# Optimization experiments

Measured on AMD Instinct MI355X. Metric: run time of the kernel, lower is better.

Reference implementation:

```python
import jax, jax.numpy as jnp
import numpy as np

D_MODEL = 1024
NUM_HEADS = 16


def setup_inputs() -> dict:
    key = jax.random.key(0)
    kx, kq, kk, kv, ko = jax.random.split(key, 5)
    B, S, D = 4, 2048, D_MODEL
    scale = 0.02
    x = jax.random.normal(kx, (B, S, D), dtype=jnp.float32)
    wq = jax.random.normal(kq, (D, D), dtype=jnp.float32) * scale
    wk = jax.random.normal(kk, (D, D), dtype=jnp.float32) * scale
    wv = jax.random.normal(kv, (D, D), dtype=jnp.float32) * scale
    wo = jax.random.normal(ko, (D, D), dtype=jnp.float32) * scale
    return {"x": x, "wq": wq, "wk": wk, "wv": wv, "wo": wo}


def reference(x, wq, wk, wv, wo):
    B, S, D = x.shape
    H = NUM_HEADS
    dk = D // H
    # projections: weight is [out, in] -> y = x @ W^T
    q = jnp.einsum('bsd,ed->bse', x, wq).reshape(B, S, H, dk).transpose(0, 2, 1, 3)
    k = jnp.einsum('bsd,ed->bse', x, wk).reshape(B, S, H, dk).transpose(0, 2, 1, 3)
    v = jnp.einsum('bsd,ed->bse', x, wv).reshape(B, S, H, dk).transpose(0, 2, 1, 3)
    # scaled dot-product attention with causal mask, [B,H,S,S]
    scores = jnp.einsum('bhqd,bhkd->bhqk', q, k) / jnp.sqrt(jnp.asarray(dk, x.dtype))
    causal = jnp.tril(jnp.ones((S, S), dtype=bool))
    scores = jnp.where(causal, scores, -jnp.inf)
    attn = jax.nn.softmax(scores, axis=-1)
    out = jnp.einsum('bhqk,bhkd->bhqd', attn, v)
    out = out.transpose(0, 2, 1, 3).reshape(B, S, D)
    return jnp.einsum('bse,de->bsd', out, wo)
```

## Files before the change

### kernel.cpp

```cpp
#include <hip/hip_runtime.h>

#define SEQ 2048
#define DM 1024
#define NH 16
#define DKH 64

typedef __attribute__((ext_vector_type(8))) short short8;
typedef __attribute__((ext_vector_type(4))) float f32x4;

static __device__ __forceinline__ unsigned short f2b(float f) {
  unsigned int u = __float_as_uint(f);
  u += 0x7fffu + ((u >> 16) & 1u);
  return (unsigned short)(u >> 16);
}

static __device__ __forceinline__ short8 ldfrag_bf(const unsigned short* p) {
  return *reinterpret_cast<const short8*>(p);
}
static __device__ __forceinline__ short8 ldfrag_f32(const float* p) {
  const float4* q = reinterpret_cast<const float4*>(p);
  float4 a = q[0], b = q[1];
  short8 r;
  r[0] = (short)f2b(a.x); r[1] = (short)f2b(a.y);
  r[2] = (short)f2b(a.z); r[3] = (short)f2b(a.w);
  r[4] = (short)f2b(b.x); r[5] = (short)f2b(b.y);
  r[6] = (short)f2b(b.z); r[7] = (short)f2b(b.w);
  return r;
}

static __device__ __forceinline__ void gl_lds16(const void* g, void* l) {
  __builtin_amdgcn_global_load_lds(
      (const __attribute__((address_space(1))) unsigned int*)g,
      (__attribute__((address_space(3))) unsigned int*)l, 16, 0, 0);
}

__global__ __launch_bounds__(256) void zero_f32(float* __restrict__ p, int n4) {
  int i = blockIdx.x * 256 + threadIdx.x;
  if (i < n4) {
    float4 z = {0.f, 0.f, 0.f, 0.f};
    reinterpret_cast<float4*>(p)[i] = z;
  }
}

__global__ __launch_bounds__(256) void cast_f32_bf16(const float* __restrict__ src,
                                                     unsigned short* __restrict__ dst,
                                                     int n4) {
  int i = blockIdx.x * 256 + threadIdx.x;
  if (i < n4) {
    float4 v = reinterpret_cast<const float4*>(src)[i];
    ushort4 o;
    o.x = f2b(v.x); o.y = f2b(v.y); o.z = f2b(v.z); o.w = f2b(v.w);
    reinterpret_cast<ushort4*>(dst)[i] = o;
  }
}

__global__ __launch_bounds__(256) void cast4_w(const float* __restrict__ a, const float* __restrict__ b,
                                               const float* __restrict__ c, const float* __restrict__ d,
                                               unsigned short* __restrict__ oa, unsigned short* __restrict__ ob,
                                               unsigned short* __restrict__ oc, unsigned short* __restrict__ od) {
  int which = blockIdx.x >> 10;
  int i = (blockIdx.x & 1023) * 256 + threadIdx.x;
  const float* s = (which == 0) ? a : (which == 1) ? b : (which == 2) ? c : d;
  unsigned short* o = (which == 0) ? oa : (which == 1) ? ob : (which == 2) ? oc : od;
  float sc = (which == 0) ? 0.125f : 1.0f;
  float4 v = reinterpret_cast<const float4*>(s)[i];
  ushort4 u;
  u.x = f2b(v.x * sc); u.y = f2b(v.y * sc); u.z = f2b(v.z * sc); u.w = f2b(v.w * sc);
  reinterpret_cast<ushort4*>(o)[i] = u;
}

__global__ __launch_bounds__(256) void gemm_qkv(const unsigned short* __restrict__ A,
                                                const unsigned short* __restrict__ Wq,
                                                const unsigned short* __restrict__ Wk,
                                                const unsigned short* __restrict__ Wv,
                                                unsigned short* __restrict__ Qb,
                                                unsigned short* __restrict__ Kb,
                                                unsigned short* __restrict__ Vt) {
  __shared__ char smem[32768];
  unsigned short* At = (unsigned short*)smem;
  unsigned short* Wt = (unsigned short*)(smem + 16384);
  int t = threadIdx.x;
  int lane = t & 63;
  int w = t >> 6;
  int l16 = lane & 15, q4 = lane >> 4;
  int mode = blockIdx.x % 3;
  int bid = blockIdx.x / 3;
  int mt = bid >> 3, nt = bid & 7;
  int m0 = mt * 128, n0 = nt * 128;
  int mw = (w & 1) * 64, nw = (w >> 1) * 64;
  const unsigned short* W = (mode == 0) ? Wq : (mode == 1) ? Wk : Wv;

  const f32x4 zero4 = {0.f, 0.f, 0.f, 0.f};
  f32x4 acc[4][4];
#pragma unroll
  for (int mi = 0; mi < 4; ++mi)
#pragma unroll
    for (int nj = 0; nj < 4; ++nj) acc[mi][nj] = zero4;

  int rl0 = t >> 2, cp = t & 3;
  const unsigned short* ga0 = A + (long)(m0 + rl0) * DM + ((cp - rl0) & 3) * 8;
  const unsigned short* ga1 = A + (long)(m0 + rl0 + 64) * DM + ((cp - (rl0 + 64)) & 3) * 8;
  const unsigned short* gw0 = W + (long)(n0 + rl0) * DM + ((cp - rl0) & 3) * 8;
  const unsigned short* gw1 = W + (long)(n0 + rl0 + 64) * DM + ((cp - (rl0 + 64)) & 3) * 8;
  char* lA = (char*)At + t * 16;
  char* lW = (char*)Wt + t * 16;

  int aoff[4], woff[4];
#pragma unroll
  for (int mi = 0; mi < 4; ++mi) {
    int r = mw + mi * 16 + l16;
    aoff[mi] = r * 32 + ((q4 + r) & 3) * 8;
  }
#pragma unroll
  for (int nj = 0; nj < 4; ++nj) {
    int r = nw + nj * 16 + l16;
    woff[nj] = r * 32 + ((q4 + r) & 3) * 8;
  }

  gl_lds16(ga0, lA); gl_lds16(ga1, lA + 4096);
  gl_lds16(gw0, lW); gl_lds16(gw1, lW + 4096);

  for (int ks = 0; ks < 32; ++ks) {
    __syncthreads();
    if (ks + 1 < 32) {
      ga0 += 32; ga1 += 32; gw0 += 32; gw1 += 32;
      int bo = ((ks + 1) & 1) * 8192;
      gl_lds16(ga0, lA + bo); gl_lds16(ga1, lA + bo + 4096);
      gl_lds16(gw0, lW + bo); gl_lds16(gw1, lW + bo + 4096);
    }
    const unsigned short* Ab = At + (ks & 1) * 4096;
    const unsigned short* Wb = Wt + (ks & 1) * 4096;

    short8 af[4], wf[4];
#pragma unroll
    for (int mi = 0; mi < 4; ++mi) af[mi] = ldfrag_bf(Ab + aoff[mi]);
#pragma unroll
    for (int nj = 0; nj < 4; ++nj) wf[nj] = ldfrag_bf(Wb + woff[nj]);
#pragma unroll
    for (int mi = 0; mi < 4; ++mi)
#pragma unroll
      for (int nj = 0; nj < 4; ++nj)
        acc[mi][nj] = __builtin_amdgcn_mfma_f32_16x16x32_bf16(af[mi], wf[nj], acc[mi][nj], 0, 0, 0);
  }

  if (mode != 2) {
    unsigned short* o = (mode == 0) ? Qb : Kb;
#pragma unroll
    for (int mi = 0; mi < 4; ++mi)
#pragma unroll
      for (int nj = 0; nj < 4; ++nj)
#pragma unroll
        for (int r = 0; r < 4; ++r) {
          int m = m0 + mw + mi * 16 + q4 * 4 + r;
          int n = n0 + nw + nj * 16 + l16;
          int b = m >> 11, s = m & 2047;
          int h = n >> 6, d = n & 63;
          long bh = (long)(b * NH + h);
          o[(bh * SEQ + s) * DKH + d] = f2b(acc[mi][nj][r]);
        }
  } else {
    __syncthreads();
    unsigned short* vle = (unsigned short*)(smem + w * 8192);
    unsigned int* vle32 = (unsigned int*)vle;
#pragma unroll
    for (int nj = 0; nj < 4; ++nj) {
      int d = nj * 16 + l16;
      int k8 = (d & 7) * 8;
#pragma unroll
      for (int mi = 0; mi < 4; ++mi)
#pragma unroll
        for (int r = 0; r < 4; r += 2) {
          int s = mi * 16 + q4 * 4 + r;
          unsigned int pk = (unsigned int)f2b(acc[mi][nj][r]) |
                            ((unsigned int)f2b(acc[mi][nj][r + 1]) << 16);
          vle32[d * 32 + ((s ^ k8) >> 1)] = pk;
        }
    }
    __asm__ volatile("s_waitcnt lgkmcnt(0)" ::: "memory");
    int b = m0 >> 11;
    int h = (n0 + nw) >> 6;
    long bh = (long)(b * NH + h);
    int sbase = (m0 + mw) & 2047;
    int dr_lo = lane >> 3, c = lane & 7;
#pragma unroll
    for (int pass = 0; pass < 8; ++pass) {
      int dr = pass * 8 + dr_lo;
      int cc = c ^ (dr & 7);
      short8 vv = ldfrag_bf(vle + dr * 64 + cc * 8);
      *reinterpret_cast<short8*>(Vt + (bh * DKH + dr) * SEQ + sbase + c * 8) = vv;
    }
  }
}

__global__ __launch_bounds__(256) void gemm_o(const unsigned short* __restrict__ A,
                                              const unsigned short* __restrict__ W,
                                              float* __restrict__ outp) {
  __shared__ char smem[32768];
  unsigned short* At = (unsigned short*)smem;
  unsigned short* Wt = (unsigned short*)(smem + 16384);
  int t = threadIdx.x;
  int lane = t & 63;
  int w = t >> 6;
  int l16 = lane & 15, q4 = lane >> 4;
  int mt = blockIdx.x >> 3, nt = blockIdx.x & 7;
  int m0 = mt * 128, n0 = nt * 128;
  int mw = (w & 1) * 64, nw = (w >> 1) * 64;

  const f32x4 zero4 = {0.f, 0.f, 0.f, 0.f};
  f32x4 acc[4][4];
#pragma unroll
  for (int mi = 0; mi < 4; ++mi)
#pragma unroll
    for (int nj = 0; nj < 4; ++nj) acc[mi][nj] = zero4;

  int rl0 = t >> 2, cp = t & 3;
  int b0 = m0 >> 11;
  const unsigned short* ga0;
  const unsigned short* ga1;
  {
    int s0 = (m0 & 2047) + rl0;
    ga0 = A + (long)b0 * (NH * SEQ * DKH) + (long)s0 * DKH + ((cp - rl0) & 3) * 8;
    int s1 = (m0 & 2047) + rl0 + 64;
    ga1 = A + (long)b0 * (NH * SEQ * DKH) + (long)s1 * DKH + ((cp - (rl0 + 64)) & 3) * 8;
  }
  const unsigned short* gw0 = W + (long)(n0 + rl0) * DM + ((cp - rl0) & 3) * 8;
  const unsigned short* gw1 = W + (long)(n0 + rl0 + 64) * DM + ((cp - (rl0 + 64)) & 3) * 8;
  char* lA = (char*)At + t * 16;
  char* lW = (char*)Wt + t * 16;

  int aoff[4], woff[4];
#pragma unroll
  for (int mi = 0; mi < 4; ++mi) {
    int r = mw + mi * 16 + l16;
    aoff[mi] = r * 32 + ((q4 + r) & 3) * 8;
  }
#pragma unroll
  for (int nj = 0; nj < 4; ++nj) {
    int r = nw + nj * 16 + l16;
    woff[nj] = r * 32 + ((q4 + r) & 3) * 8;
  }

  gl_lds16(ga0, lA); gl_lds16(ga1, lA + 4096);
  gl_lds16(gw0, lW); gl_lds16(gw1, lW + 4096);

  for (int ks = 0; ks < 32; ++ks) {
    __syncthreads();
    if (ks + 1 < 32) {
      int adv = ((ks & 1) == 0) ? 32 : (SEQ * DKH - 32);
      ga0 += adv; ga1 += adv; gw0 += 32; gw1 += 32;
      int bo = ((ks + 1) & 1) * 8192;
      gl_lds16(ga0, lA + bo); gl_lds16(ga1, lA + bo + 4096);
      gl_lds16(gw0, lW + bo); gl_lds16(gw1, lW + bo + 4096);
    }
    const unsigned short* Ab = At + (ks & 1) * 4096;
    const unsigned short* Wb = Wt + (ks & 1) * 4096;

    short8 af[4], wf[4];
#pragma unroll
    for (int mi = 0; mi < 4; ++mi) af[mi] = ldfrag_bf(Ab + aoff[mi]);
#pragma unroll
    for (int nj = 0; nj < 4; ++nj) wf[nj] = ldfrag_bf(Wb + woff[nj]);
#pragma unroll
    for (int mi = 0; mi < 4; ++mi)
#pragma unroll
      for (int nj = 0; nj < 4; ++nj)
        acc[mi][nj] = __builtin_amdgcn_mfma_f32_16x16x32_bf16(af[mi], wf[nj], acc[mi][nj], 0, 0, 0);
  }

#pragma unroll
  for (int mi = 0; mi < 4; ++mi)
#pragma unroll
    for (int nj = 0; nj < 4; ++nj)
#pragma unroll
      for (int r = 0; r < 4; ++r) {
        int m = m0 + mw + mi * 16 + q4 * 4 + r;
        int n = n0 + nw + nj * 16 + l16;
        outp[(long)m * DM + n] = acc[mi][nj][r];
      }
}

template<int MODE, bool AF32, bool WF32>
__global__ __launch_bounds__(256) void gemm_s(const void* __restrict__ Ap,
                                              const void* __restrict__ Wp,
                                              void* __restrict__ outp) {
  int wid  = (blockIdx.x * 256 + threadIdx.x) >> 6;
  int lane = threadIdx.x & 63;
  int l16  = lane & 15, q4 = lane >> 4;
  int tn = wid & 15, tm = wid >> 4;
  int m0 = tm * 32, n0 = tn * 64;

  const float*          Af = (const float*)Ap;
  const unsigned short* Ab = (const unsigned short*)Ap;
  const float*          Wf = (const float*)Wp;
  const unsigned short* Wb = (const unsigned short*)Wp;

  const f32x4 zero4 = {0.f, 0.f, 0.f, 0.f};
  f32x4 acc[2][4];
#pragma unroll
  for (int mi = 0; mi < 2; ++mi)
#pragma unroll
    for (int j = 0; j < 4; ++j) acc[mi][j] = zero4;

  int wrow[4];
#pragma unroll
  for (int j = 0; j < 4; ++j) wrow[j] = (n0 + j * 16 + l16) * DM;
  int arow[2] = {0, 0};
  long abase[2] = {0, 0};
  if (MODE != 3) {
#pragma unroll
    for (int mi = 0; mi < 2; ++mi) arow[mi] = (m0 + mi * 16 + l16) * DM;
  } else {
    int b = m0 >> 11;
#pragma unroll
    for (int mi = 0; mi < 2; ++mi) {
      int srow = (m0 & 2047) + mi * 16 + l16;
      abase[mi] = (long)b * (NH * SEQ * DKH) + (long)srow * DKH;
    }
  }

#pragma unroll 2
  for (int ks = 0; ks < 32; ++ks) {
    int ko = ks * 32 + q4 * 8;
    short8 bfrag[4];
#pragma unroll
    for (int j = 0; j < 4; ++j) {
      if constexpr (WF32) bfrag[j] = ldfrag_f32(Wf + wrow[j] + ko);
      else                bfrag[j] = ldfrag_bf(Wb + wrow[j] + ko);
    }
    short8 afrag[2];
    if constexpr (MODE != 3) {
#pragma unroll
      for (int mi = 0; mi < 2; ++mi) {
        if constexpr (AF32) afrag[mi] = ldfrag_f32(Af + arow[mi] + ko);
        else                afrag[mi] = ldfrag_bf(Ab + arow[mi] + ko);
      }
    } else {
      int h = ko >> 6, e63 = ko & 63;
#pragma unroll
      for (int mi = 0; mi < 2; ++mi)
        afrag[mi] = ldfrag_bf(Ab + abase[mi] + (long)h * (SEQ * DKH) + e63);
    }
#pragma unroll
    for (int mi = 0; mi < 2; ++mi)
#pragma unroll
      for (int j = 0; j < 4; ++j)
        acc[mi][j] = __builtin_amdgcn_mfma_f32_16x16x32_bf16(afrag[mi], bfrag[j], acc[mi][j], 0, 0, 0);
  }

#pragma unroll
  for (int mi = 0; mi < 2; ++mi) {
#pragma unroll
    for (int j = 0; j < 4; ++j) {
#pragma unroll
      for (int r = 0; r < 4; ++r) {
        float v = acc[mi][j][r];
        int m = m0 + mi * 16 + q4 * 4 + r;
        int n = n0 + j * 16 + l16;
        if constexpr (MODE == 3) {
          reinterpret_cast<float*>(outp)[(long)m * DM + n] = v;
        } else {
          int b = m >> 11, s = m & 2047;
          int h = n >> 6, d = n & 63;
          long bh = (long)(b * NH + h);
          unsigned short* o = reinterpret_cast<unsigned short*>(outp);
          if constexpr (MODE == 0)      o[(bh * SEQ + s) * DKH + d] = f2b(v * 0.125f);
          else if constexpr (MODE == 1) o[(bh * SEQ + s) * DKH + d] = f2b(v);
          else                          o[(bh * DKH + d) * SEQ + s] = f2b(v);
        }
      }
    }
  }
}

#define PSTR 72
__global__ __launch_bounds__(256) void attn_k(const unsigned short* __restrict__ Kbuf,
                                              const unsigned short* __restrict__ Vt,
                                              const unsigned short* __restrict__ Qbuf,
                                              unsigned short* __restrict__ Obuf) {
  __shared__ unsigned short Kt[2][64 * 64];
  __shared__ unsigned short Vts[2][64 * 64];
  __shared__ unsigned short Pl[4][32 * PSTR];

  int t = threadIdx.x;
  int lane = t & 63;
  int w = t >> 6;
  int l16 = lane & 15, q4 = lane >> 4;
  int qb = 15 - (blockIdx.x >> 6);
  int bh = blockIdx.x & 63;
  int q0 = qb * 128;
  int qw0 = q0 + w * 32;

  const unsigned short* Qh = Qbuf + (long)bh * (SEQ * DKH);
  const unsigned short* Kh = Kbuf + (long)bh * (SEQ * DKH);
  const unsigned short* Vh = Vt   + (long)bh * (DKH * SEQ);
  unsigned short* pl = Pl[w];

  short8 qf[2][2];
#pragma unroll
  for (int mi = 0; mi < 2; ++mi)
#pragma unroll
    for (int c = 0; c < 2; ++c)
      qf[mi][c] = ldfrag_bf(Qh + (qw0 + mi * 16 + l16) * DKH + c * 32 + q4 * 8);

  short8 onef;
#pragma unroll
  for (int j = 0; j < 8; ++j) onef[j] = (short)0x3F80;

  const f32x4 zero4 = {0.f, 0.f, 0.f, 0.f};
  f32x4 om[2][4], lsum[2];
#pragma unroll
  for (int mi = 0; mi < 2; ++mi) {
    lsum[mi] = zero4;
#pragma unroll
    for (int c = 0; c < 4; ++c) om[mi][c] = zero4;
  }

  int koff[4][2], voff[4][2];
#pragma unroll
  for (int tt = 0; tt < 4; ++tt) {
    int kr = tt * 16 + l16;
#pragma unroll
    for (int c = 0; c < 2; ++c) koff[tt][c] = kr * 64 + ((c * 4 + q4 + kr) & 7) * 8;
  }
#pragma unroll
  for (int c = 0; c < 4; ++c) {
    int dr = c * 16 + l16;
#pragma unroll
    for (int half = 0; half < 2; ++half) voff[c][half] = dr * 64 + ((half * 4 + q4 + dr) & 7) * 8;
  }

  int rl0 = t >> 3, cp = t & 7;
  const unsigned short* kp0 = Kh + (long)rl0 * DKH + ((cp - rl0) & 7) * 8;
  const unsigned short* kp1 = Kh + (long)(rl0 + 32) * DKH + ((cp - (rl0 + 32)) & 7) * 8;
  const unsigned short* vp0 = Vh + (long)rl0 * SEQ + ((cp - rl0) & 7) * 8;
  const unsigned short* vp1 = Vh + (long)(rl0 + 32) * SEQ + ((cp - (rl0 + 32)) & 7) * 8;
  char* lK = (char*)Kt + t * 16;
  char* lV = (char*)Vts + t * 16;

  int nk = 2 * qb + 2;
  gl_lds16(kp0, lK); gl_lds16(kp1, lK + 4096);
  gl_lds16(vp0, lV); gl_lds16(vp1, lV + 4096);

  for (int it = 0; it < nk; ++it) {
    __syncthreads();
    if (it + 1 < nk) {
      kp0 += 64 * DKH; kp1 += 64 * DKH; vp0 += 64; vp1 += 64;
      int bo = ((it + 1) & 1) * 8192;
      gl_lds16(kp0, lK + bo); gl_lds16(kp1, lK + bo + 4096);
      gl_lds16(vp0, lV + bo); gl_lds16(vp1, lV + bo + 4096);
    }

    int k0 = it * 64;
    if (k0 <= qw0 + 31) {
      const unsigned short* KT = Kt[0] + (it & 1) * 4096;
      const unsigned short* VT = Vts[0] + (it & 1) * 4096;
      bool needmask = (k0 + 63 > qw0);

      f32x4 s[2][4];
#pragma unroll
      for (int mi = 0; mi < 2; ++mi)
#pragma unroll
        for (int tt = 0; tt < 4; ++tt) s[mi][tt] = zero4;
#pragma unroll
      for (int tt = 0; tt < 4; ++tt) {
#pragma unroll
        for (int c = 0; c < 2; ++c) {
          short8 kf = ldfrag_bf(KT + koff[tt][c]);
#pragma unroll
          for (int mi = 0; mi < 2; ++mi)
            s[mi][tt] = __builtin_amdgcn_mfma_f32_16x16x32_bf16(qf[mi][c], kf, s[mi][tt], 0, 0, 0);
        }
      }
#pragma unroll
      for (int mi = 0; mi < 2; ++mi)
#pragma unroll
        for (int tt = 0; tt < 4; ++tt) {
          int key = k0 + tt * 16 + l16;
#pragma unroll
          for (int r = 0; r < 4; ++r) {
            float p;
            if (needmask) {
              int qrow = qw0 + mi * 16 + q4 * 4 + r;
              p = (key <= qrow) ? __expf(s[mi][tt][r]) : 0.f;
            } else {
              p = __expf(s[mi][tt][r]);
            }
            pl[(mi * 16 + q4 * 4 + r) * PSTR + tt * 16 + l16] =
                (unsigned short)(__float_as_uint(p) >> 16);
          }
        }
      __asm__ volatile("s_waitcnt lgkmcnt(0)" ::: "memory");
#pragma unroll
      for (int half = 0; half < 2; ++half) {
        short8 pa[2];
#pragma unroll
        for (int mi = 0; mi < 2; ++mi) {
          pa[mi] = ldfrag_bf(pl + (mi * 16 + l16) * PSTR + half * 32 + q4 * 8);
          lsum[mi] = __builtin_amdgcn_mfma_f32_16x16x32_bf16(pa[mi], onef, lsum[mi], 0, 0, 0);
        }
#pragma unroll
        for (int c = 0; c < 4; ++c) {
          short8 vf = ldfrag_bf(VT + voff[c][half]);
#pragma unroll
          for (int mi = 0; mi < 2; ++mi)
            om[mi][c] = __builtin_amdgcn_mfma_f32_16x16x32_bf16(pa[mi], vf, om[mi][c], 0, 0, 0);
        }
      }
    }
  }

#pragma unroll
  for (int mi = 0; mi < 2; ++mi) {
    float inv[4];
#pragma unroll
    for (int r = 0; r < 4; ++r) inv[r] = 1.f / lsum[mi][r];
#pragma unroll
    for (int c = 0; c < 4; ++c)
#pragma unroll
      for (int r = 0; r < 4; ++r) {
        int row = qw0 + mi * 16 + q4 * 4 + r;
        Obuf[(long)bh * (SEQ * DKH) + row * DKH + c * 16 + l16] = f2b(om[mi][c][r] * inv[r]);
      }
  }
}

extern "C" void kernel_launch(void* const* d_in, const int* in_sizes, int n_in,
                              void* d_out, int out_size, void* d_ws, size_t ws_size,
                              hipStream_t stream) {
  const float* x  = (const float*)d_in[0];
  const float* wq = (const float*)d_in[1];
  const float* wk = (const float*)d_in[2];
  const float* wv = (const float*)d_in[3];
  const float* wo = (const float*)d_in[4];

  unsigned short* Qb = (unsigned short*)d_out;
  unsigned short* Kb = Qb + 8388608;

  if (ws_size >= 41943040ull) {
    unsigned short* xb  = (unsigned short*)d_ws;
    unsigned short* wqb = xb + 8388608;
    unsigned short* wkb = wqb + 1048576;
    unsigned short* wvb = wkb + 1048576;
    unsigned short* wob = wvb + 1048576;
    unsigned short* Vt  = wob + 1048576;
    unsigned short* Ob  = xb;

    cast_f32_bf16<<<8192, 256, 0, stream>>>(x, xb, 2097152);
    cast4_w<<<4096, 256, 0, stream>>>(wq, wk, wv, wo, wqb, wkb, wvb, wob);

    gemm_qkv<<<1536, 256, 0, stream>>>(xb, wqb, wkb, wvb, Qb, Kb, Vt);
    attn_k<<<1024, 256, 0, stream>>>(Kb, Vt, Qb, Ob);
    gemm_o<<<512, 256, 0, stream>>>(Ob, wob, (float*)d_out);
  } else if (ws_size >= 33554432ull) {
    unsigned short* Vt = (unsigned short*)d_ws;
    unsigned short* Ob = Vt + 8388608;

    gemm_s<0, true, true><<<1024, 256, 0, stream>>>(x, wq, Qb);
    gemm_s<1, true, true><<<1024, 256, 0, stream>>>(x, wk, Kb);
    gemm_s<2, true, true><<<1024, 256, 0, stream>>>(x, wv, Vt);
    attn_k<<<1024, 256, 0, stream>>>(Kb, Vt, Qb, Ob);
    gemm_s<3, false, true><<<1024, 256, 0, stream>>>(Ob, wo, d_out);
  } else {
    zero_f32<<<8192, 256, 0, stream>>>((float*)d_out, 2097152);
  }
}
```

Before: 270.4 us.

## Merge cast kernels and load V fragments directly from global in attention

Result: slower. 309.2 us (+14.3%).

```diff
diff --git a/kernel.cpp b/kernel.cpp
--- a/kernel.cpp
+++ b/kernel.cpp
@@ -54,19 +54,30 @@
   }
 }
 
-__global__ __launch_bounds__(256) void cast4_w(const float* __restrict__ a, const float* __restrict__ b,
-                                               const float* __restrict__ c, const float* __restrict__ d,
-                                               unsigned short* __restrict__ oa, unsigned short* __restrict__ ob,
-                                               unsigned short* __restrict__ oc, unsigned short* __restrict__ od) {
-  int which = blockIdx.x >> 10;
-  int i = (blockIdx.x & 1023) * 256 + threadIdx.x;
-  const float* s = (which == 0) ? a : (which == 1) ? b : (which == 2) ? c : d;
-  unsigned short* o = (which == 0) ? oa : (which == 1) ? ob : (which == 2) ? oc : od;
-  float sc = (which == 0) ? 0.125f : 1.0f;
-  float4 v = reinterpret_cast<const float4*>(s)[i];
-  ushort4 u;
-  u.x = f2b(v.x * sc); u.y = f2b(v.y * sc); u.z = f2b(v.z * sc); u.w = f2b(v.w * sc);
-  reinterpret_cast<ushort4*>(o)[i] = u;
+__global__ __launch_bounds__(256) void cast_all(const float* __restrict__ x,
+                                                const float* __restrict__ a, const float* __restrict__ b,
+                                                const float* __restrict__ c, const float* __restrict__ d,
+                                                unsigned short* __restrict__ ox,
+                                                unsigned short* __restrict__ oa, unsigned short* __restrict__ ob,
+                                                unsigned short* __restrict__ oc, unsigned short* __restrict__ od) {
+  if (blockIdx.x < 8192) {
+    int i = blockIdx.x * 256 + threadIdx.x;
+    float4 v = reinterpret_cast<const float4*>(x)[i];
+    ushort4 u;
+    u.x = f2b(v.x); u.y = f2b(v.y); u.z = f2b(v.z); u.w = f2b(v.w);
+    reinterpret_cast<ushort4*>(ox)[i] = u;
+  } else {
+    int wb = blockIdx.x - 8192;
+    int which = wb >> 10;
+    int i = (wb & 1023) * 256 + threadIdx.x;
+    const float* s = (which == 0) ? a : (which == 1) ? b : (which == 2) ? c : d;
+    unsigned short* o = (which == 0) ? oa : (which == 1) ? ob : (which == 2) ? oc : od;
+    float sc = (which == 0) ? 0.125f : 1.0f;
+    float4 v = reinterpret_cast<const float4*>(s)[i];
+    ushort4 u;
+    u.x = f2b(v.x * sc); u.y = f2b(v.y * sc); u.z = f2b(v.z * sc); u.w = f2b(v.w * sc);
+    reinterpret_cast<ushort4*>(o)[i] = u;
+  }
 }
 
 __global__ __launch_bounds__(256) void gemm_qkv(const unsigned short* __restrict__ A,
@@ -378,7 +389,6 @@
                                               const unsigned short* __restrict__ Qbuf,
                                               unsigned short* __restrict__ Obuf) {
   __shared__ unsigned short Kt[2][64 * 64];
-  __shared__ unsigned short Vts[2][64 * 64];
   __shared__ unsigned short Pl[4][32 * PSTR];
 
   int t = threadIdx.x;
@@ -415,45 +425,36 @@
     for (int c = 0; c < 4; ++c) om[mi][c] = zero4;
   }
 
-  int koff[4][2], voff[4][2];
+  int koff[4][2];
 #pragma unroll
   for (int tt = 0; tt < 4; ++tt) {
     int kr = tt * 16 + l16;
 #pragma unroll
     for (int c = 0; c < 2; ++c) koff[tt][c] = kr * 64 + ((c * 4 + q4 + kr) & 7) * 8;
   }
-#pragma unroll
-  for (int c = 0; c < 4; ++c) {
-    int dr = c * 16 + l16;
-#pragma unroll
-    for (int half = 0; half < 2; ++half) voff[c][half] = dr * 64 + ((half * 4 + q4 + dr) & 7) * 8;
-  }
+  const unsigned short* vbase[4];
+#pragma unroll
+  for (int c = 0; c < 4; ++c) vbase[c] = Vh + (long)(c * 16 + l16) * SEQ + q4 * 8;
 
   int rl0 = t >> 3, cp = t & 7;
   const unsigned short* kp0 = Kh + (long)rl0 * DKH + ((cp - rl0) & 7) * 8;
   const unsigned short* kp1 = Kh + (long)(rl0 + 32) * DKH + ((cp - (rl0 + 32)) & 7) * 8;
-  const unsigned short* vp0 = Vh + (long)rl0 * SEQ + ((cp - rl0) & 7) * 8;
-  const unsigned short* vp1 = Vh + (long)(rl0 + 32) * SEQ + ((cp - (rl0 + 32)) & 7) * 8;
   char* lK = (char*)Kt + t * 16;
-  char* lV = (char*)Vts + t * 16;
 
   int nk = 2 * qb + 2;
   gl_lds16(kp0, lK); gl_lds16(kp1, lK + 4096);
-  gl_lds16(vp0, lV); gl_lds16(vp1, lV + 4096);
 
   for (int it = 0; it < nk; ++it) {
     __syncthreads();
     if (it + 1 < nk) {
-      kp0 += 64 * DKH; kp1 += 64 * DKH; vp0 += 64; vp1 += 64;
+      kp0 += 64 * DKH; kp1 += 64 * DKH;
       int bo = ((it + 1) & 1) * 8192;
       gl_lds16(kp0, lK + bo); gl_lds16(kp1, lK + bo + 4096);
-      gl_lds16(vp0, lV + bo); gl_lds16(vp1, lV + bo + 4096);
     }
 
     int k0 = it * 64;
     if (k0 <= qw0 + 31) {
       const unsigned short* KT = Kt[0] + (it & 1) * 4096;
-      const unsigned short* VT = Vts[0] + (it & 1) * 4096;
       bool needmask = (k0 + 63 > qw0);
 
       f32x4 s[2][4];
@@ -500,7 +501,7 @@
         }
 #pragma unroll
         for (int c = 0; c < 4; ++c) {
-          short8 vf = ldfrag_bf(VT + voff[c][half]);
+          short8 vf = ldfrag_bf(vbase[c] + k0 + half * 32);
 #pragma unroll
           for (int mi = 0; mi < 2; ++mi)
             om[mi][c] = __builtin_amdgcn_mfma_f32_16x16x32_bf16(pa[mi], vf, om[mi][c], 0, 0, 0);
@@ -545,8 +546,7 @@
     unsigned short* Vt  = wob + 1048576;
     unsigned short* Ob  = xb;
 
-    cast_f32_bf16<<<8192, 256, 0, stream>>>(x, xb, 2097152);
-    cast4_w<<<4096, 256, 0, stream>>>(wq, wk, wv, wo, wqb, wkb, wvb, wob);
+    cast_all<<<12288, 256, 0, stream>>>(x, wq, wk, wv, wo, xb, wqb, wkb, wvb, wob);
 
     gemm_qkv<<<1536, 256, 0, stream>>>(xb, wqb, wkb, wvb, Qb, Kb, Vt);
     attn_k<<<1024, 256, 0, stream>>>(Kb, Vt, Qb, Ob);
```
